# Kernel optimization log

Hardware: AMD Instinct MI355X
Metric: run time of the kernel (lower is better)

## Reference

```python
import jax, jax.numpy as jnp
import numpy as np

N_NODES = 30000
N_EDGES = 480000
EMB_DIM = 512
NUM_REL = 4
VOCAB = 64


def setup_inputs() -> dict:
    key = jax.random.key(0)
    ks = jax.random.split(key, 14)

    def nrm(k, shape):
        return jax.random.normal(k, shape, dtype=jnp.float32) * 0.05

    return {
        "x_idx": jax.random.randint(ks[0], (N_NODES, 1), 0, VOCAB),
        "edge_index": jax.random.randint(ks[1], (2, N_EDGES), 0, N_NODES),
        "edge_type": jax.random.randint(ks[2], (N_EDGES,), 0, NUM_REL),
        "emb": nrm(ks[3], (VOCAB, EMB_DIM)),
        "W1": nrm(ks[4], (NUM_REL, EMB_DIM, EMB_DIM)),
        "root1": nrm(ks[5], (EMB_DIM, EMB_DIM)),
        "b1": jnp.zeros((EMB_DIM,), jnp.float32),
        "W2": nrm(ks[6], (NUM_REL, EMB_DIM, EMB_DIM)),
        "root2": nrm(ks[7], (EMB_DIM, EMB_DIM)),
        "b2": jnp.zeros((EMB_DIM,), jnp.float32),
        "W3": nrm(ks[8], (NUM_REL, EMB_DIM, EMB_DIM)),
        "root3": nrm(ks[9], (EMB_DIM, EMB_DIM)),
        "b3": jnp.zeros((EMB_DIM,), jnp.float32),
    }


def rgcn_conv(x, src, dst, etype, W, Wroot, b):
    # PyG RGCNConv semantics: per-relation MEAN aggregation of neighbor
    # features, transformed by relation weight, plus root transform + bias.
    # Aggregate-then-transform is mathematically identical to per-edge
    # transform (mean is linear) but needs only R dense GEMMs.
    R = W.shape[0]
    Nn, Dd = x.shape
    seg = etype * Nn + dst  # combined (relation, dst) segment id
    msg_sum = jax.ops.segment_sum(x[src], seg, num_segments=R * Nn)
    msg_sum = msg_sum.reshape(R, Nn, Dd)  # [R, N, D]
    cnt = jax.ops.segment_sum(jnp.ones((src.shape[0],), x.dtype), seg,
                              num_segments=R * Nn).reshape(R, Nn, 1)
    mean = msg_sum / jnp.maximum(cnt, 1.0)  # zero rows stay zero
    out = jnp.einsum('rnd,rde->ne', mean, W)  # relation-specific transform
    return out + x @ Wroot + b


def reference(x_idx, edge_index, edge_type, emb,
              W1, root1, b1, W2, root2, b2, W3, root3, b3):
    src, dst = edge_index[0], edge_index[1]
    x = emb[x_idx[:, 0]]  # [N, D] embedding lookup (squeeze(-1))
    x = jax.nn.relu(rgcn_conv(x, src, dst, edge_type, W1, root1, b1)) + x
    x = jax.nn.relu(rgcn_conv(x, src, dst, edge_type, W2, root2, b2)) + x
    x = jax.nn.relu(rgcn_conv(x, src, dst, edge_type, W3, root3, b3)) + x
    return x
```

## Files before the change

### kernel.cpp

```cpp
#include <hip/hip_runtime.h>
#include <hip/hip_bf16.h>

#define N_NODES 30000
#define N_EDGES 480000
#define DIM 512
#define NREL 4
#define NSEG (NREL * N_NODES)
#define KTOT ((NREL + 1) * DIM)
#define NT (KTOT / 64)
#define NBM ((N_NODES + 255) / 256)
#define NWG_GEMM (NBM * 2)

typedef __attribute__((ext_vector_type(8))) short short8;
typedef __attribute__((ext_vector_type(4))) float f32x4;

__device__ __forceinline__ float bf2f(unsigned int hi) {
    union { unsigned int u; float f; } v; v.u = hi << 16; return v.f;
}
__device__ __forceinline__ unsigned short f2bf(float f) {
    union { float f; unsigned int u; } v; v.f = f;
    unsigned int u = v.u;
    unsigned int r = (u + 0x7fffu + ((u >> 16) & 1u)) >> 16;
    return (unsigned short)r;
}

__global__ void k_wcat(const float* __restrict__ W, const float* __restrict__ root,
                       unsigned short* __restrict__ wt) {
    int i = blockIdx.x * 256 + threadIdx.x;
    if (i >= DIM * KTOT) return;
    int k = i % KTOT, e = i / KTOT;
    float v;
    if (k < DIM) {
        v = root[k * DIM + e];
    } else {
        int kk = k - DIM;
        int r = kk >> 9; kk &= 511;
        v = W[(size_t)r * DIM * DIM + (size_t)kk * DIM + e];
    }
    wt[(size_t)e * KTOT + k] = f2bf(v);
}

__global__ void k_embed(const int* __restrict__ xidx, const float* __restrict__ emb,
                        unsigned short* __restrict__ xb) {
    int n = blockIdx.x;
    int l = threadIdx.x;
    int id = xidx[n];
    const float4* er = (const float4*)(emb + (size_t)id * DIM + l * 8);
    float4 a = er[0], b = er[1];
    ushort4 pa, pb;
    pa.x = f2bf(a.x); pa.y = f2bf(a.y); pa.z = f2bf(a.z); pa.w = f2bf(a.w);
    pb.x = f2bf(b.x); pb.y = f2bf(b.y); pb.z = f2bf(b.z); pb.w = f2bf(b.w);
    ushort4* xbo = (ushort4*)(xb + (size_t)n * DIM + l * 8);
    xbo[0] = pa; xbo[1] = pb;
}

__global__ void k_hist(const int* __restrict__ etype, const int* __restrict__ dst,
                       int* __restrict__ hist) {
    int e = blockIdx.x * 256 + threadIdx.x;
    if (e < N_EDGES) atomicAdd(&hist[etype[e] * N_NODES + dst[e]], 1);
}

__global__ void k_scan1(const int* __restrict__ hist, int* __restrict__ offsets,
                        int* __restrict__ bsums) {
    __shared__ int sdata[256];
    int t = threadIdx.x, b = blockIdx.x;
    int base = b * 2048 + t * 8;
    int v[8]; int s = 0;
    #pragma unroll
    for (int i = 0; i < 8; i++) {
        int idx = base + i;
        v[i] = (idx < NSEG) ? hist[idx] : 0;
        s += v[i];
    }
    sdata[t] = s; __syncthreads();
    for (int off = 1; off < 256; off <<= 1) {
        int x = (t >= off) ? sdata[t - off] : 0;
        __syncthreads();
        sdata[t] += x;
        __syncthreads();
    }
    int run = (t == 0) ? 0 : sdata[t - 1];
    #pragma unroll
    for (int i = 0; i < 8; i++) {
        run += v[i];
        int idx = base + i;
        if (idx < NSEG) offsets[idx + 1] = run;
    }
    if (t == 255) bsums[b] = sdata[255];
}

__global__ void k_scan2(int* __restrict__ bsums, int nb) {
    if (threadIdx.x == 0 && blockIdx.x == 0) {
        int run = 0;
        for (int i = 0; i < nb; i++) { int v = bsums[i]; bsums[i] = run; run += v; }
    }
}

__global__ void k_scan3(const int* __restrict__ bsums, int* __restrict__ offsets) {
    int t = threadIdx.x, b = blockIdx.x;
    int base = b * 2048 + t * 8;
    int add = bsums[b];
    #pragma unroll
    for (int i = 0; i < 8; i++) {
        int idx = base + i;
        if (idx < NSEG) offsets[idx + 1] += add;
    }
    if (b == 0 && t == 0) offsets[0] = 0;
}

__global__ void k_scatter(const int* __restrict__ etype, const int* __restrict__ src,
                          const int* __restrict__ dst, const int* __restrict__ offsets,
                          int* __restrict__ cursor, int* __restrict__ ssrc) {
    int e = blockIdx.x * 256 + threadIdx.x;
    if (e < N_EDGES) {
        int seg = etype[e] * N_NODES + dst[e];
        int p = atomicAdd(&cursor[seg], 1);
        ssrc[offsets[seg] + p] = src[e];
    }
}

__global__ __launch_bounds__(256) void k_agg(const unsigned short* __restrict__ xb,
                                             const int* __restrict__ ssrc,
                                             const int* __restrict__ offsets,
                                             unsigned short* __restrict__ meanb) {
    int wid = threadIdx.x >> 6, lane = threadIdx.x & 63;
    int seg = blockIdx.x * 4 + wid;
    int st = offsets[seg], en = offsets[seg + 1];
    float acc[8] = {0, 0, 0, 0, 0, 0, 0, 0};
    for (int i = st; i < en; i++) {
        int s = ssrc[i];
        uint4 v = *(const uint4*)(xb + (size_t)s * DIM + lane * 8);
        acc[0] += bf2f(v.x & 0xffffu); acc[1] += bf2f(v.x >> 16);
        acc[2] += bf2f(v.y & 0xffffu); acc[3] += bf2f(v.y >> 16);
        acc[4] += bf2f(v.z & 0xffffu); acc[5] += bf2f(v.z >> 16);
        acc[6] += bf2f(v.w & 0xffffu); acc[7] += bf2f(v.w >> 16);
    }
    float inv = (en > st) ? 1.0f / (float)(en - st) : 0.0f;
    uint4 o;
    o.x = (unsigned int)f2bf(acc[0] * inv) | ((unsigned int)f2bf(acc[1] * inv) << 16);
    o.y = (unsigned int)f2bf(acc[2] * inv) | ((unsigned int)f2bf(acc[3] * inv) << 16);
    o.z = (unsigned int)f2bf(acc[4] * inv) | ((unsigned int)f2bf(acc[5] * inv) << 16);
    o.w = (unsigned int)f2bf(acc[6] * inv) | ((unsigned int)f2bf(acc[7] * inv) << 16);
    *(uint4*)(meanb + (size_t)seg * DIM + lane * 8) = o;
}


#define GLD16(g, l)                                                                     \
    __builtin_amdgcn_global_load_lds((const __attribute__((address_space(1))) void*)(g), \
                                     (__attribute__((address_space(3))) void*)(l), 16, 0, 0)

#define STAGE_A(tile, ksh, bufo) do {                                                   \
    int _pt = (tile) >> 3;                                                              \
    const unsigned short* _ab = (_pt == 0) ? xb : meanb + (size_t)(_pt - 1) * N_NODES * DIM; \
    int _kc = (((tile) & 7) << 6) + ((ksh) << 5) + gcol;                                \
    int _g0 = m0 + srow; if (_g0 >= N_NODES) _g0 = 0;                                   \
    int _g1 = m0 + srow + 128; if (_g1 >= N_NODES) _g1 = 0;                             \
    GLD16(_ab + (size_t)_g0 * DIM + _kc, S + (bufo) + ((ksh) * 8192) + (wid << 9));     \
    GLD16(_ab + (size_t)_g1 * DIM + _kc, S + (bufo) + ((ksh) * 8192) + 4096 + (wid << 9)); \
} while (0)

#define STAGE_B(tile, ksh, bufo) do {                                                   \
    int _kc = ((tile) << 6) + ((ksh) << 5) + gcol;    \
    const unsigned short* _w0 = wt + (size_t)(n0 + srow) * KTOT + _kc;                  \
    GLD16(_w0, S + (bufo) + 16384 + ((ksh) * 8192) + (wid << 9));                       \
    GLD16(_w0 + (size_t)128 * KTOT, S + (bufo) + 16384 + ((ksh) * 8192) + 4096 + (wid << 9)); \
} while (0)

#define READ_A(mq, ks, bufo) do {                                                       \
    const unsigned short* _ap = S + (bufo) + (ks) * 8192 + arowF + (mq) * 2048 + cofs;  \
    a[0] = *(const short8*)(_ap);                                                       \
    a[1] = *(const short8*)(_ap + 512);                                                 \
    a[2] = *(const short8*)(_ap + 1024);                                                \
    a[3] = *(const short8*)(_ap + 1536);                                                \
} while (0)

#define READ_B(ks, bufo) do {                                                           \
    const unsigned short* _bp = S + (bufo) + 16384 + (ks) * 8192 + brow0 + cofs;        \
    b[0] = *(const short8*)(_bp);                                                       \
    b[1] = *(const short8*)(_bp + 512);                                                 \
    b[2] = *(const short8*)(_bp + 1024);                                                \
    b[3] = *(const short8*)(_bp + 1536);                                                \
} while (0)

#define MFMA16(mq) do {                                                                 \
    _Pragma("unroll") for (int _m = 0; _m < 4; ++_m)                                    \
    _Pragma("unroll") for (int _n = 0; _n < 4; ++_n)                                    \
        acc[(mq) * 4 + _m][_n] =                                                        \
            __builtin_amdgcn_mfma_f32_16x16x32_bf16(a[_m], b[_n], acc[(mq) * 4 + _m][_n], 0, 0, 0); \
} while (0)

#define PH_TOP()  __builtin_amdgcn_s_barrier();                                         \
                  asm volatile("s_waitcnt lgkmcnt(0)" ::: "memory");                    \
                  __builtin_amdgcn_sched_barrier(0);                                    \
                  __builtin_amdgcn_s_setprio(1)
#define PH_BOT()  __builtin_amdgcn_s_setprio(0); __builtin_amdgcn_sched_barrier(0);     \
                  __builtin_amdgcn_s_barrier()
#define VMC6()    asm volatile("s_waitcnt vmcnt(6)" ::: "memory")
#define VMC0()    asm volatile("s_waitcnt vmcnt(0)" ::: "memory")

__global__ __launch_bounds__(512, 2) void k_gemm(const unsigned short* __restrict__ xb,
                                                 const unsigned short* __restrict__ meanb,
                                                 const unsigned short* __restrict__ wt,
                                                 const float* __restrict__ bias,
                                                 float* __restrict__ outf,
                                                 unsigned short* __restrict__ xbn,
                                                 int wf32, int wbf16) {
    extern __shared__ unsigned short S[];
    int tid = threadIdx.x;
    int lane = tid & 63, wid = tid >> 6;

    int orig = blockIdx.x;
    int xcd = orig & 7, tix = orig >> 3;
    const int q = NWG_GEMM >> 3, r = NWG_GEMM & 7;
    int wgid = (xcd < r ? xcd * (q + 1) : r * (q + 1) + (xcd - r) * q) + tix;
    int bn = wgid & 1, bm = wgid >> 1;
    int m0 = bm * 256, n0 = bn * 256;
    int wm = wid >> 2, wn = wid & 3;

    int r15 = lane & 15, c4 = lane >> 4;
    int f = (r15 + (r15 >> 2)) & 3;
    int cofs = ((c4 ^ f) << 3);
    int arowF = (wm * 128 + r15) * 32;
    int brow0 = (wn * 64 + r15) * 32;

    int srow = tid >> 2;
    int f_t = (srow + (srow >> 2)) & 3;
    int gcol = (((tid & 3) ^ f_t) << 3);

    short8 a[4], b[4];
    f32x4 acc[8][4] = {};

    STAGE_B(0, 0, 0); STAGE_A(0, 0, 0); STAGE_B(0, 1, 0); STAGE_A(0, 1, 0);
    STAGE_B(1, 0, 32768); STAGE_A(1, 0, 32768); STAGE_B(1, 1, 32768);
    VMC6();
    __builtin_amdgcn_s_barrier();

    for (int it = 0; it < NT / 2; ++it) {
        int t1 = 2 * it + 1, t2 = 2 * it + 2, t3 = 2 * it + 3;
        READ_A(0, 0, 0); READ_B(0, 0);
        STAGE_A(t1, 1, 32768);
        PH_TOP(); MFMA16(0); PH_BOT();
        READ_A(1, 0, 0);
        if (t2 < NT) STAGE_B(t2, 0, 0);
        PH_TOP(); MFMA16(1); PH_BOT();
        READ_A(0, 1, 0); READ_B(1, 0);
        if (t2 < NT) STAGE_A(t2, 0, 0);
        PH_TOP(); MFMA16(0); PH_BOT();
        READ_A(1, 1, 0);
        if (t2 < NT) { STAGE_B(t2, 1, 0); VMC6(); } else { VMC0(); }
        PH_TOP(); MFMA16(1); PH_BOT();
        READ_A(0, 0, 32768); READ_B(0, 32768);
        if (t2 < NT) STAGE_A(t2, 1, 0);
        PH_TOP(); MFMA16(0); PH_BOT();
        READ_A(1, 0, 32768);
        if (t3 < NT) STAGE_B(t3, 0, 32768);
        PH_TOP(); MFMA16(1); PH_BOT();
        READ_A(0, 1, 32768); READ_B(1, 32768);
        if (t3 < NT) STAGE_A(t3, 0, 32768);
        PH_TOP(); MFMA16(0); PH_BOT();
        READ_A(1, 1, 32768);
        if (t3 < NT) { STAGE_B(t3, 1, 32768); VMC6(); } else { VMC0(); }
        PH_TOP(); MFMA16(1); PH_BOT();
    }
    VMC0();

    #pragma unroll
    for (int mm = 0; mm < 8; ++mm) {
        int rowoff = ((mm >> 2) << 6) + ((mm & 3) << 4);
        #pragma unroll
        for (int j = 0; j < 4; ++j) {
            int row = m0 + wm * 128 + rowoff + c4 * 4 + j;
            if (row >= N_NODES) continue;
            #pragma unroll
            for (int n = 0; n < 4; ++n) {
                int col = n0 + wn * 64 + n * 16 + r15;
                float v = acc[mm][n][j] + bias[col];
                v = fmaxf(v, 0.0f) + bf2f(xb[(size_t)row * DIM + col]);
                if (wf32)  outf[(size_t)row * DIM + col] = v;
                if (wbf16) xbn[(size_t)row * DIM + col] = f2bf(v);
            }
        }
    }
}

extern "C" void kernel_launch(void* const* d_in, const int* in_sizes, int n_in,
                              void* d_out, int out_size, void* d_ws, size_t ws_size,
                              hipStream_t stream) {
    const int* xidx   = (const int*)d_in[0];
    const int* eidx   = (const int*)d_in[1];
    const int* etype  = (const int*)d_in[2];
    const float* emb  = (const float*)d_in[3];
    const float* Wl[3]    = {(const float*)d_in[4], (const float*)d_in[7], (const float*)d_in[10]};
    const float* rootl[3] = {(const float*)d_in[5], (const float*)d_in[8], (const float*)d_in[11]};
    const float* bl[3]    = {(const float*)d_in[6], (const float*)d_in[9], (const float*)d_in[12]};
    const int* esrc = eidx;
    const int* edst = eidx + N_EDGES;

    char* ws = (char*)d_ws;
    size_t off = 0;
    auto take = [&](size_t bytes) { char* p = ws + off; off = (off + bytes + 255) & ~(size_t)255; return p; };
    unsigned short* xb0  = (unsigned short*)take((size_t)N_NODES * DIM * 2);
    unsigned short* xb1  = (unsigned short*)take((size_t)N_NODES * DIM * 2);
    unsigned short* meanb= (unsigned short*)take((size_t)NREL * N_NODES * DIM * 2);
    unsigned short* wcat = (unsigned short*)take((size_t)3 * DIM * KTOT * 2);
    int* hist    = (int*)take((size_t)NSEG * 4);
    int* offsets = (int*)take((size_t)(NSEG + 1) * 4);
    int* cursor  = (int*)take((size_t)NSEG * 4);
    int* bsums   = (int*)take(64 * 4);
    int* ssrc    = (int*)take((size_t)N_EDGES * 4);

    hipMemsetAsync(hist, 0, (size_t)NSEG * 4, stream);
    hipMemsetAsync(cursor, 0, (size_t)NSEG * 4, stream);
    for (int l = 0; l < 3; l++) {
        k_wcat<<<(DIM * KTOT + 255) / 256, 256, 0, stream>>>(Wl[l], rootl[l],
                                                             wcat + (size_t)l * DIM * KTOT);
    }
    k_embed<<<N_NODES, 64, 0, stream>>>(xidx, emb, xb0);
    k_hist<<<(N_EDGES + 255) / 256, 256, 0, stream>>>(etype, edst, hist);
    k_scan1<<<(NSEG + 2047) / 2048, 256, 0, stream>>>(hist, offsets, bsums);
    k_scan2<<<1, 64, 0, stream>>>(bsums, (NSEG + 2047) / 2048);
    k_scan3<<<(NSEG + 2047) / 2048, 256, 0, stream>>>(bsums, offsets);
    k_scatter<<<(N_EDGES + 255) / 256, 256, 0, stream>>>(etype, esrc, edst, offsets, cursor, ssrc);

    unsigned short* xb_cur = xb0;
    unsigned short* xb_nxt = xb1;
    for (int l = 0; l < 3; l++) {
        k_agg<<<N_NODES, 256, 0, stream>>>(xb_cur, ssrc, offsets, meanb);
        int last = (l == 2);
        k_gemm<<<NWG_GEMM, 512, 131072, stream>>>(xb_cur, meanb, wcat + (size_t)l * DIM * KTOT,
                                                  bl[l], (float*)d_out, xb_nxt,
                                                  last ? 1 : 0, last ? 0 : 1);
        unsigned short* t = xb_cur; xb_cur = xb_nxt; xb_nxt = t;
    }
}
```

Measured before the change: 656.3 us.

## Merge GEMM phases into 32-MFMA blocks and unroll aggregation loop by two

The GEMM main loop is restructured from eight 16-MFMA phases per iteration into four 32-MFMA phases. Each phase reads eight A fragments and issues A and B stage loads together, with the vmcnt wait threshold changed from 6 to 4. This halves the number of barrier/setprio phase boundaries, but raises register pressure from holding eight A fragments and changes how far ahead loads are issued. The aggregation kernel also processes two neighbor rows per iteration to put more gather loads in flight.

```diff
diff --git a/kernel.cpp b/kernel.cpp
--- a/kernel.cpp
+++ b/kernel.cpp
@@ -127,7 +127,21 @@
     int seg = blockIdx.x * 4 + wid;
     int st = offsets[seg], en = offsets[seg + 1];
     float acc[8] = {0, 0, 0, 0, 0, 0, 0, 0};
-    for (int i = st; i < en; i++) {
+    int i = st;
+    for (; i + 1 < en; i += 2) {
+        int s0 = ssrc[i], s1 = ssrc[i + 1];
+        uint4 v0 = *(const uint4*)(xb + (size_t)s0 * DIM + lane * 8);
+        uint4 v1 = *(const uint4*)(xb + (size_t)s1 * DIM + lane * 8);
+        acc[0] += bf2f(v0.x & 0xffffu) + bf2f(v1.x & 0xffffu);
+        acc[1] += bf2f(v0.x >> 16)     + bf2f(v1.x >> 16);
+        acc[2] += bf2f(v0.y & 0xffffu) + bf2f(v1.y & 0xffffu);
+        acc[3] += bf2f(v0.y >> 16)     + bf2f(v1.y >> 16);
+        acc[4] += bf2f(v0.z & 0xffffu) + bf2f(v1.z & 0xffffu);
+        acc[5] += bf2f(v0.z >> 16)     + bf2f(v1.z >> 16);
+        acc[6] += bf2f(v0.w & 0xffffu) + bf2f(v1.w & 0xffffu);
+        acc[7] += bf2f(v0.w >> 16)     + bf2f(v1.w >> 16);
+    }
+    if (i < en) {
         int s = ssrc[i];
         uint4 v = *(const uint4*)(xb + (size_t)s * DIM + lane * 8);
         acc[0] += bf2f(v.x & 0xffffu); acc[1] += bf2f(v.x >> 16);
@@ -152,7 +166,7 @@
 #define STAGE_A(tile, ksh, bufo) do {                                                   \
     int _pt = (tile) >> 3;                                                              \
     const unsigned short* _ab = (_pt == 0) ? xb : meanb + (size_t)(_pt - 1) * N_NODES * DIM; \
-    int _kc = (((tile) & 7) << 6) + ((ksh) << 5) + gcol;                                \
+    int _kc = (((tile) & 7) << 6) + ((ksh) << 5) + gcol;         \
     int _g0 = m0 + srow; if (_g0 >= N_NODES) _g0 = 0;                                   \
     int _g1 = m0 + srow + 128; if (_g1 >= N_NODES) _g1 = 0;                             \
     GLD16(_ab + (size_t)_g0 * DIM + _kc, S + (bufo) + ((ksh) * 8192) + (wid << 9));     \
@@ -160,18 +174,22 @@
 } while (0)
 
 #define STAGE_B(tile, ksh, bufo) do {                                                   \
-    int _kc = ((tile) << 6) + ((ksh) << 5) + gcol;    \
+    int _kc = ((tile) << 6) + ((ksh) << 5) + gcol;                  \
     const unsigned short* _w0 = wt + (size_t)(n0 + srow) * KTOT + _kc;                  \
     GLD16(_w0, S + (bufo) + 16384 + ((ksh) * 8192) + (wid << 9));                       \
     GLD16(_w0 + (size_t)128 * KTOT, S + (bufo) + 16384 + ((ksh) * 8192) + 4096 + (wid << 9)); \
 } while (0)
 
-#define READ_A(mq, ks, bufo) do {                                                       \
-    const unsigned short* _ap = S + (bufo) + (ks) * 8192 + arowF + (mq) * 2048 + cofs;  \
+#define READ_A8(ks, bufo) do {                                                          \
+    const unsigned short* _ap = S + (bufo) + (ks) * 8192 + arowF + cofs;                \
     a[0] = *(const short8*)(_ap);                                                       \
     a[1] = *(const short8*)(_ap + 512);                                                 \
     a[2] = *(const short8*)(_ap + 1024);                                                \
     a[3] = *(const short8*)(_ap + 1536);                                                \
+    a[4] = *(const short8*)(_ap + 2048);                                                \
+    a[5] = *(const short8*)(_ap + 2560);                                                \
+    a[6] = *(const short8*)(_ap + 3072);                                                \
+    a[7] = *(const short8*)(_ap + 3584);                                                \
 } while (0)
 
 #define READ_B(ks, bufo) do {                                                           \
@@ -182,11 +200,11 @@
     b[3] = *(const short8*)(_bp + 1536);                                                \
 } while (0)
 
-#define MFMA16(mq) do {                                                                 \
-    _Pragma("unroll") for (int _m = 0; _m < 4; ++_m)                                    \
+#define MFMA32() do {                                                                   \
+    _Pragma("unroll") for (int _m = 0; _m < 8; ++_m)                                    \
     _Pragma("unroll") for (int _n = 0; _n < 4; ++_n)                                    \
-        acc[(mq) * 4 + _m][_n] =                                                        \
-            __builtin_amdgcn_mfma_f32_16x16x32_bf16(a[_m], b[_n], acc[(mq) * 4 + _m][_n], 0, 0, 0); \
+        acc[_m][_n] =                                                                   \
+            __builtin_amdgcn_mfma_f32_16x16x32_bf16(a[_m], b[_n], acc[_m][_n], 0, 0, 0); \
 } while (0)
 
 #define PH_TOP()  __builtin_amdgcn_s_barrier();                                         \
@@ -195,8 +213,9 @@
                   __builtin_amdgcn_s_setprio(1)
 #define PH_BOT()  __builtin_amdgcn_s_setprio(0); __builtin_amdgcn_sched_barrier(0);     \
                   __builtin_amdgcn_s_barrier()
-#define VMC6()    asm volatile("s_waitcnt vmcnt(6)" ::: "memory")
+#define VMC4()    asm volatile("s_waitcnt vmcnt(4)" ::: "memory")
 #define VMC0()    asm volatile("s_waitcnt vmcnt(0)" ::: "memory")
+#define BUF1 32768
 
 __global__ __launch_bounds__(512, 2) void k_gemm(const unsigned short* __restrict__ xb,
                                                  const unsigned short* __restrict__ meanb,
@@ -227,40 +246,29 @@
     int f_t = (srow + (srow >> 2)) & 3;
     int gcol = (((tid & 3) ^ f_t) << 3);
 
-    short8 a[4], b[4];
+    short8 a[8], b[4];
     f32x4 acc[8][4] = {};
 
-    STAGE_B(0, 0, 0); STAGE_A(0, 0, 0); STAGE_B(0, 1, 0); STAGE_A(0, 1, 0);
-    STAGE_B(1, 0, 32768); STAGE_A(1, 0, 32768); STAGE_B(1, 1, 32768);
-    VMC6();
+    STAGE_A(0, 0, 0);    STAGE_B(0, 0, 0);
+    STAGE_A(0, 1, 0);    STAGE_B(0, 1, 0);
+    STAGE_A(1, 0, BUF1); STAGE_B(1, 0, BUF1);
+    VMC4();
     __builtin_amdgcn_s_barrier();
 
     for (int it = 0; it < NT / 2; ++it) {
         int t1 = 2 * it + 1, t2 = 2 * it + 2, t3 = 2 * it + 3;
-        READ_A(0, 0, 0); READ_B(0, 0);
-        STAGE_A(t1, 1, 32768);
-        PH_TOP(); MFMA16(0); PH_BOT();
-        READ_A(1, 0, 0);
-        if (t2 < NT) STAGE_B(t2, 0, 0);
-        PH_TOP(); MFMA16(1); PH_BOT();
-        READ_A(0, 1, 0); READ_B(1, 0);
-        if (t2 < NT) STAGE_A(t2, 0, 0);
-        PH_TOP(); MFMA16(0); PH_BOT();
-        READ_A(1, 1, 0);
-        if (t2 < NT) { STAGE_B(t2, 1, 0); VMC6(); } else { VMC0(); }
-        PH_TOP(); MFMA16(1); PH_BOT();
-        READ_A(0, 0, 32768); READ_B(0, 32768);
-        if (t2 < NT) STAGE_A(t2, 1, 0);
-        PH_TOP(); MFMA16(0); PH_BOT();
-        READ_A(1, 0, 32768);
-        if (t3 < NT) STAGE_B(t3, 0, 32768);
-        PH_TOP(); MFMA16(1); PH_BOT();
-        READ_A(0, 1, 32768); READ_B(1, 32768);
-        if (t3 < NT) STAGE_A(t3, 0, 32768);
-        PH_TOP(); MFMA16(0); PH_BOT();
-        READ_A(1, 1, 32768);
-        if (t3 < NT) { STAGE_B(t3, 1, 32768); VMC6(); } else { VMC0(); }
-        PH_TOP(); MFMA16(1); PH_BOT();
+        READ_A8(0, 0); READ_B(0, 0);
+        STAGE_A(t1, 1, BUF1); STAGE_B(t1, 1, BUF1);
+        PH_TOP(); MFMA32(); PH_BOT();
+        READ_A8(1, 0); READ_B(1, 0);
+        if (t2 < NT) { STAGE_A(t2, 0, 0); STAGE_B(t2, 0, 0); VMC4(); } else { VMC0(); }
+        PH_TOP(); MFMA32(); PH_BOT();
+        READ_A8(0, BUF1); READ_B(0, BUF1);
+        if (t2 < NT) { STAGE_A(t2, 1, 0); STAGE_B(t2, 1, 0); }
+        PH_TOP(); MFMA32(); PH_BOT();
+        READ_A8(1, BUF1); READ_B(1, BUF1);
+        if (t3 < NT) { STAGE_A(t3, 0, BUF1); STAGE_B(t3, 0, BUF1); VMC4(); } else { VMC0(); }
+        PH_TOP(); MFMA32(); PH_BOT();
     }
     VMC0();
 
```

New measurement: 659.1 us. Within noise of the previous version (+0.4%).

## Rework GEMM staging schedule, unroll aggregation by two, pack embed blocks

Applied to the files above, without the earlier changes.

The GEMM main loop gets a new order for staging the A and B tiles. The barrier at the end of each phase is removed and the vmcnt waits are placed differently, so that global-to-LDS loads overlap more with the MFMA work and fewer barriers run per step. The aggregation kernel now processes two neighbor rows per iteration, which puts more loads in flight, and the embed kernel runs four nodes per 256-thread block. Removing the bottom barrier risks LDS read/write hazards between waves if the new wait placement does not fully cover buffer reuse.

```diff
diff --git a/kernel.cpp b/kernel.cpp
--- a/kernel.cpp
+++ b/kernel.cpp
@@ -42,8 +42,9 @@
 
 __global__ void k_embed(const int* __restrict__ xidx, const float* __restrict__ emb,
                         unsigned short* __restrict__ xb) {
-    int n = blockIdx.x;
-    int l = threadIdx.x;
+    int n = blockIdx.x * 4 + (threadIdx.x >> 6);
+    int l = threadIdx.x & 63;
+    if (n >= N_NODES) return;
     int id = xidx[n];
     const float4* er = (const float4*)(emb + (size_t)id * DIM + l * 8);
     float4 a = er[0], b = er[1];
@@ -127,7 +128,21 @@
     int seg = blockIdx.x * 4 + wid;
     int st = offsets[seg], en = offsets[seg + 1];
     float acc[8] = {0, 0, 0, 0, 0, 0, 0, 0};
-    for (int i = st; i < en; i++) {
+    int i = st;
+    for (; i + 1 < en; i += 2) {
+        int s0 = ssrc[i], s1 = ssrc[i + 1];
+        uint4 v0 = *(const uint4*)(xb + (size_t)s0 * DIM + lane * 8);
+        uint4 v1 = *(const uint4*)(xb + (size_t)s1 * DIM + lane * 8);
+        acc[0] += bf2f(v0.x & 0xffffu) + bf2f(v1.x & 0xffffu);
+        acc[1] += bf2f(v0.x >> 16)     + bf2f(v1.x >> 16);
+        acc[2] += bf2f(v0.y & 0xffffu) + bf2f(v1.y & 0xffffu);
+        acc[3] += bf2f(v0.y >> 16)     + bf2f(v1.y >> 16);
+        acc[4] += bf2f(v0.z & 0xffffu) + bf2f(v1.z & 0xffffu);
+        acc[5] += bf2f(v0.z >> 16)     + bf2f(v1.z >> 16);
+        acc[6] += bf2f(v0.w & 0xffffu) + bf2f(v1.w & 0xffffu);
+        acc[7] += bf2f(v0.w >> 16)     + bf2f(v1.w >> 16);
+    }
+    if (i < en) {
         int s = ssrc[i];
         uint4 v = *(const uint4*)(xb + (size_t)s * DIM + lane * 8);
         acc[0] += bf2f(v.x & 0xffffu); acc[1] += bf2f(v.x >> 16);
@@ -152,7 +167,7 @@
 #define STAGE_A(tile, ksh, bufo) do {                                                   \
     int _pt = (tile) >> 3;                                                              \
     const unsigned short* _ab = (_pt == 0) ? xb : meanb + (size_t)(_pt - 1) * N_NODES * DIM; \
-    int _kc = (((tile) & 7) << 6) + ((ksh) << 5) + gcol;                                \
+    int _kc = (((tile) & 7) << 6) + ((ksh) << 5) + gcol;         \
     int _g0 = m0 + srow; if (_g0 >= N_NODES) _g0 = 0;                                   \
     int _g1 = m0 + srow + 128; if (_g1 >= N_NODES) _g1 = 0;                             \
     GLD16(_ab + (size_t)_g0 * DIM + _kc, S + (bufo) + ((ksh) * 8192) + (wid << 9));     \
@@ -160,7 +175,7 @@
 } while (0)
 
 #define STAGE_B(tile, ksh, bufo) do {                                                   \
-    int _kc = ((tile) << 6) + ((ksh) << 5) + gcol;    \
+    int _kc = ((tile) << 6) + ((ksh) << 5) + gcol;                  \
     const unsigned short* _w0 = wt + (size_t)(n0 + srow) * KTOT + _kc;                  \
     GLD16(_w0, S + (bufo) + 16384 + ((ksh) * 8192) + (wid << 9));                       \
     GLD16(_w0 + (size_t)128 * KTOT, S + (bufo) + 16384 + ((ksh) * 8192) + 4096 + (wid << 9)); \
@@ -193,10 +208,11 @@
                   asm volatile("s_waitcnt lgkmcnt(0)" ::: "memory");                    \
                   __builtin_amdgcn_sched_barrier(0);                                    \
                   __builtin_amdgcn_s_setprio(1)
-#define PH_BOT()  __builtin_amdgcn_s_setprio(0); __builtin_amdgcn_sched_barrier(0);     \
-                  __builtin_amdgcn_s_barrier()
+#define PH_BOT()  __builtin_amdgcn_s_setprio(0); __builtin_amdgcn_sched_barrier(0)
 #define VMC6()    asm volatile("s_waitcnt vmcnt(6)" ::: "memory")
+#define VMC4()    asm volatile("s_waitcnt vmcnt(4)" ::: "memory")
 #define VMC0()    asm volatile("s_waitcnt vmcnt(0)" ::: "memory")
+#define BUF1 32768
 
 __global__ __launch_bounds__(512, 2) void k_gemm(const unsigned short* __restrict__ xb,
                                                  const unsigned short* __restrict__ meanb,
@@ -231,35 +247,36 @@
     f32x4 acc[8][4] = {};
 
     STAGE_B(0, 0, 0); STAGE_A(0, 0, 0); STAGE_B(0, 1, 0); STAGE_A(0, 1, 0);
-    STAGE_B(1, 0, 32768); STAGE_A(1, 0, 32768); STAGE_B(1, 1, 32768);
-    VMC6();
+    STAGE_B(1, 0, BUF1); STAGE_A(1, 0, BUF1);
+    VMC4();
     __builtin_amdgcn_s_barrier();
 
     for (int it = 0; it < NT / 2; ++it) {
         int t1 = 2 * it + 1, t2 = 2 * it + 2, t3 = 2 * it + 3;
         READ_A(0, 0, 0); READ_B(0, 0);
-        STAGE_A(t1, 1, 32768);
+        STAGE_B(t1, 1, BUF1);
         PH_TOP(); MFMA16(0); PH_BOT();
         READ_A(1, 0, 0);
-        if (t2 < NT) STAGE_B(t2, 0, 0);
+        VMC6();
         PH_TOP(); MFMA16(1); PH_BOT();
         READ_A(0, 1, 0); READ_B(1, 0);
-        if (t2 < NT) STAGE_A(t2, 0, 0);
+        STAGE_A(t1, 1, BUF1);
+        if (t2 < NT) STAGE_B(t2, 0, 0);
         PH_TOP(); MFMA16(0); PH_BOT();
         READ_A(1, 1, 0);
-        if (t2 < NT) { STAGE_B(t2, 1, 0); VMC6(); } else { VMC0(); }
+        if (t2 < NT) { STAGE_A(t2, 0, 0); VMC6(); } else { VMC0(); }
         PH_TOP(); MFMA16(1); PH_BOT();
-        READ_A(0, 0, 32768); READ_B(0, 32768);
-        if (t2 < NT) STAGE_A(t2, 1, 0);
+        READ_A(0, 0, BUF1); READ_B(0, BUF1);
+        if (t2 < NT) STAGE_B(t2, 1, 0);
         PH_TOP(); MFMA16(0); PH_BOT();
-        READ_A(1, 0, 32768);
-        if (t3 < NT) STAGE_B(t3, 0, 32768);
+        READ_A(1, 0, BUF1);
+        if (t2 < NT) { STAGE_A(t2, 1, 0); VMC6(); } else { VMC0(); }
         PH_TOP(); MFMA16(1); PH_BOT();
-        READ_A(0, 1, 32768); READ_B(1, 32768);
-        if (t3 < NT) STAGE_A(t3, 0, 32768);
+        READ_A(0, 1, BUF1); READ_B(1, BUF1);
+        if (t3 < NT) STAGE_B(t3, 0, BUF1);
         PH_TOP(); MFMA16(0); PH_BOT();
-        READ_A(1, 1, 32768);
-        if (t3 < NT) { STAGE_B(t3, 1, 32768); VMC6(); } else { VMC0(); }
+        READ_A(1, 1, BUF1);
+        if (t3 < NT) { STAGE_A(t3, 0, BUF1); VMC6(); } else { VMC0(); }
         PH_TOP(); MFMA16(1); PH_BOT();
     }
     VMC0();
@@ -315,7 +332,7 @@
         k_wcat<<<(DIM * KTOT + 255) / 256, 256, 0, stream>>>(Wl[l], rootl[l],
                                                              wcat + (size_t)l * DIM * KTOT);
     }
-    k_embed<<<N_NODES, 64, 0, stream>>>(xidx, emb, xb0);
+    k_embed<<<(N_NODES + 3) / 4, 256, 0, stream>>>(xidx, emb, xb0);
     k_hist<<<(N_EDGES + 255) / 256, 256, 0, stream>>>(etype, edst, hist);
     k_scan1<<<(NSEG + 2047) / 2048, 256, 0, stream>>>(hist, offsets, bsums);
     k_scan2<<<1, 64, 0, stream>>>(bsums, (NSEG + 2047) / 2048);
```

Measured after the change: 620.2 us. -5.5%, faster.
